# Performance work log

Measured on AMD Instinct MI355X. Metric: run time of the kernel, lower is better.

The kernel has to match this reference:

```python
import jax, jax.numpy as jnp
import numpy as np

B, L, D = 32, 256, 512
MAX_DUR = 8.0
MAX_LEN = int(L * MAX_DUR)  # static upper bound on expanded length (round(u<8) <= 8)


def setup_inputs() -> dict:
    key = jax.random.key(0)
    k1, k2 = jax.random.split(key)
    att_out = jax.random.normal(k1, (B, L, D), dtype=jnp.float32)
    # predicted per-phoneme durations in frames (float, gets rounded inside)
    duration = jax.random.uniform(k2, (B, L), dtype=jnp.float32, minval=0.0, maxval=MAX_DUR)
    return {"att_out": att_out, "duration": duration, "alpha": 1}


def reference(att_out, duration, alpha):
    # r[b,l] = number of times phoneme l is repeated (torch.round = half-to-even, same as jnp.round)
    r = jnp.round(duration * alpha).astype(jnp.int32)                 # [B, L]
    csum = jnp.cumsum(r, axis=1)                                      # [B, L] cumulative end offsets
    total = csum[:, -1]                                               # [B] valid length per batch
    pos = jnp.arange(MAX_LEN, dtype=jnp.int32)                        # [T]
    # output frame t comes from phoneme index = first l with csum[l] > t
    idx = jax.vmap(lambda c: jnp.searchsorted(c, pos, side='right'))(csum)  # [B, T]
    idx = jnp.minimum(idx, L - 1)
    out = jnp.take_along_axis(att_out, idx[:, :, None], axis=1)       # [B, T, D] gather-expand
    mask = (pos[None, :] < total[:, None])[:, :, None]                # zero-pad like pad_sequence
    return jnp.where(mask, out, jnp.zeros((), dtype=att_out.dtype))
```

## Files before the change

### kernel.cpp

```cpp
#include <hip/hip_runtime.h>


constexpr int B = 32;
constexpr int L = 256;
constexpr int D = 512;
constexpr int MAX_LEN = 2048;
constexpr int POS_PER_BLOCK = 32;
constexpr int THREADS = 256;

typedef float vfloat4 __attribute__((ext_vector_type(4)));

__global__ __launch_bounds__(THREADS) void index_kernel(
    const float* __restrict__ duration,
    const int*   __restrict__ alpha_p,
    int*         __restrict__ idx_map)
{
    __shared__ int csum[L];
    const int b   = blockIdx.x;
    const int tid = threadIdx.x;
    const float alpha = (float)alpha_p[0];

    int v = (int)rintf(duration[b * L + tid] * alpha);
    csum[tid] = v;
    __syncthreads();
    #pragma unroll
    for (int off = 1; off < L; off <<= 1) {
        int add = (tid >= off) ? csum[tid - off] : 0;
        __syncthreads();
        csum[tid] += add;
        __syncthreads();
    }
    const int total = csum[L - 1];

    #pragma unroll
    for (int j = 0; j < MAX_LEN / THREADS; ++j) {
        const int p = tid + j * THREADS;
        int result = -1;
        if (p < total) {
            int lo = 0, hi = L;
            while (lo < hi) {
                int mid = (lo + hi) >> 1;
                if (csum[mid] <= p) lo = mid + 1; else hi = mid;
            }
            result = lo;
        }
        idx_map[b * MAX_LEN + p] = result;
    }
}

__global__ __launch_bounds__(THREADS) void copy_kernel(
    const float* __restrict__ att_out,
    const int*   __restrict__ idx_map,
    float*       __restrict__ out)
{
    const int b        = blockIdx.y;
    const int pos_base = blockIdx.x * POS_PER_BLOCK;
    const int tid      = threadIdx.x;
    const int lane     = tid & 127;
    const int row      = tid >> 7;

    const vfloat4* __restrict__ src4 = (const vfloat4*)(att_out + (size_t)b * L * D);
    vfloat4*       __restrict__ dst4 = (vfloat4*)(out + (size_t)b * MAX_LEN * D);
    const int*     __restrict__ im   = idx_map + b * MAX_LEN + pos_base;

    int ids[POS_PER_BLOCK / 2];
    #pragma unroll
    for (int i = 0; i < POS_PER_BLOCK / 2; ++i)
        ids[i] = im[2 * i + row];

    #pragma unroll
    for (int i = 0; i < POS_PER_BLOCK / 2; ++i) {
        const int p  = pos_base + 2 * i + row;
        const int id = ids[i];
        vfloat4 v = (vfloat4)0.f;
        if (id >= 0)
            v = src4[(size_t)id * (D / 4) + lane];
        dst4[(size_t)p * (D / 4) + lane] = v;
    }
}

extern "C" void kernel_launch(void* const* d_in, const int* in_sizes, int n_in,
                              void* d_out, int out_size, void* d_ws, size_t ws_size,
                              hipStream_t stream) {
    const float* att_out  = (const float*)d_in[0];
    const float* duration = (const float*)d_in[1];
    const int*   alpha    = (const int*)d_in[2];
    float*       out      = (float*)d_out;
    int*         idx_map  = (int*)d_ws;

    index_kernel<<<dim3(B), dim3(THREADS), 0, stream>>>(duration, alpha, idx_map);

    dim3 grid(MAX_LEN / POS_PER_BLOCK, B);
    copy_kernel<<<grid, dim3(THREADS), 0, stream>>>(att_out, idx_map, out);
}
```

Measured before the change: 164.9 us.

## Fuse index computation into copy kernel with wave-shuffle scan and branchless search

Merges the separate index kernel into the gather/copy kernel, so each block recomputes the per-batch cumulative durations with a single-wavefront shuffle scan and does a branchless binary search for its positions. This removes one kernel launch, the dependency between the two launches, and the idx_map round trip through global memory. The cost is redundant scan work in every block (64 blocks per batch recompute the same 256-entry prefix sum) and extra latency before the copy starts.

```diff
diff --git a/kernel.cpp b/kernel.cpp
--- a/kernel.cpp
+++ b/kernel.cpp
@@ -7,69 +7,64 @@
 constexpr int MAX_LEN = 2048;
 constexpr int POS_PER_BLOCK = 32;
 constexpr int THREADS = 256;
+constexpr int ITERS = POS_PER_BLOCK / 2;
 
 typedef float vfloat4 __attribute__((ext_vector_type(4)));
 
-__global__ __launch_bounds__(THREADS) void index_kernel(
+__global__ __launch_bounds__(THREADS) void length_regulator_kernel(
+    const float* __restrict__ att_out,
     const float* __restrict__ duration,
     const int*   __restrict__ alpha_p,
-    int*         __restrict__ idx_map)
+    float*       __restrict__ out)
 {
     __shared__ int csum[L];
-    const int b   = blockIdx.x;
-    const int tid = threadIdx.x;
-    const float alpha = (float)alpha_p[0];
 
-    int v = (int)rintf(duration[b * L + tid] * alpha);
-    csum[tid] = v;
-    __syncthreads();
-    #pragma unroll
-    for (int off = 1; off < L; off <<= 1) {
-        int add = (tid >= off) ? csum[tid - off] : 0;
-        __syncthreads();
-        csum[tid] += add;
-        __syncthreads();
-    }
-    const int total = csum[L - 1];
-
-    #pragma unroll
-    for (int j = 0; j < MAX_LEN / THREADS; ++j) {
-        const int p = tid + j * THREADS;
-        int result = -1;
-        if (p < total) {
-            int lo = 0, hi = L;
-            while (lo < hi) {
-                int mid = (lo + hi) >> 1;
-                if (csum[mid] <= p) lo = mid + 1; else hi = mid;
-            }
-            result = lo;
-        }
-        idx_map[b * MAX_LEN + p] = result;
-    }
-}
-
-__global__ __launch_bounds__(THREADS) void copy_kernel(
-    const float* __restrict__ att_out,
-    const int*   __restrict__ idx_map,
-    float*       __restrict__ out)
-{
     const int b        = blockIdx.y;
     const int pos_base = blockIdx.x * POS_PER_BLOCK;
     const int tid      = threadIdx.x;
-    const int lane     = tid & 127;
-    const int row      = tid >> 7;
+
+    if (tid < 64) {
+        const float alpha = (float)alpha_p[0];
+        vfloat4 d4 = ((const vfloat4*)(duration + b * L))[tid];
+        int r0 = (int)rintf(d4.x * alpha);
+        int r1 = (int)rintf(d4.y * alpha);
+        int r2 = (int)rintf(d4.z * alpha);
+        int r3 = (int)rintf(d4.w * alpha);
+        int s  = r0 + r1 + r2 + r3;
+        int sc = s;
+        #pragma unroll
+        for (int off = 1; off < 64; off <<= 1) {
+            int n = __shfl_up(sc, off, 64);
+            if (tid >= off) sc += n;
+        }
+        const int base = sc - s;
+        csum[4 * tid + 0] = base + r0;
+        csum[4 * tid + 1] = base + r0 + r1;
+        csum[4 * tid + 2] = base + r0 + r1 + r2;
+        csum[4 * tid + 3] = sc;
+    }
+    __syncthreads();
+
+    const int total = csum[L - 1];
+    const int lane  = tid & 127;
+    const int row   = tid >> 7;
+
+    int ids[ITERS];
+    #pragma unroll
+    for (int i = 0; i < ITERS; ++i) {
+        const int p = pos_base + 2 * i + row;
+        int idx = 0;
+        #pragma unroll
+        for (int w = 128; w >= 1; w >>= 1)
+            idx += (csum[idx + w - 1] <= p) ? w : 0;
+        ids[i] = (p < total) ? idx : -1;
+    }
 
     const vfloat4* __restrict__ src4 = (const vfloat4*)(att_out + (size_t)b * L * D);
     vfloat4*       __restrict__ dst4 = (vfloat4*)(out + (size_t)b * MAX_LEN * D);
-    const int*     __restrict__ im   = idx_map + b * MAX_LEN + pos_base;
-
-    int ids[POS_PER_BLOCK / 2];
-    #pragma unroll
-    for (int i = 0; i < POS_PER_BLOCK / 2; ++i)
-        ids[i] = im[2 * i + row];
 
     #pragma unroll
-    for (int i = 0; i < POS_PER_BLOCK / 2; ++i) {
+    for (int i = 0; i < ITERS; ++i) {
         const int p  = pos_base + 2 * i + row;
         const int id = ids[i];
         vfloat4 v = (vfloat4)0.f;
@@ -86,10 +81,7 @@
     const float* duration = (const float*)d_in[1];
     const int*   alpha    = (const int*)d_in[2];
     float*       out      = (float*)d_out;
-    int*         idx_map  = (int*)d_ws;
-
-    index_kernel<<<dim3(B), dim3(THREADS), 0, stream>>>(duration, alpha, idx_map);
 
     dim3 grid(MAX_LEN / POS_PER_BLOCK, B);
-    copy_kernel<<<grid, dim3(THREADS), 0, stream>>>(att_out, idx_map, out);
+    length_regulator_kernel<<<grid, dim3(THREADS), 0, stream>>>(att_out, duration, alpha, out);
 }
```

Result: faster. 161.2 us (-2.2%).
